# Kernel optimization log

Measured on AMD Instinct MI355X. Metric: run time of the kernel, lower is better.

## Reference

```python
import jax, jax.numpy as jnp
import numpy as np

RFF_DIM = 256
ATTENTION_SCALE = 0.1
LAMBDA_REG = 0.01
SIGMA = 1.0


def setup_inputs() -> dict:
    key = jax.random.key(0)
    k1, k2, k3 = jax.random.split(key, 3)
    N, D_IN = 262144, 64
    Z = jax.random.normal(k1, (N, D_IN), dtype=jnp.float32)
    W_rff = jax.random.normal(k2, (D_IN, RFF_DIM), dtype=jnp.float32)
    A = jax.random.normal(k3, (2 * RFF_DIM, 3), dtype=jnp.float32) * 0.01
    return {"Z": Z, "W_rff": W_rff, "A": A}


def reference(Z, W_rff, A):
    # --- RFF transform: Q = sqrt(1/R) * [cos(Z W / sigma), sin(Z W / sigma)] ---
    proj = (Z @ W_rff) / SIGMA                       # [N, R]
    Q = jnp.sqrt(1.0 / RFF_DIM) * jnp.concatenate(
        [jnp.cos(proj), jnp.sin(proj)], axis=-1)      # [N, 2R]

    N, F = Q.shape
    chunk = max(F // RFF_DIM, 1)                      # = 2 here
    n_chunks = F // chunk                             # = RFF_DIM

    # --- convexified attention over feature chunks (vectorized) ---
    Qc = Q.reshape(N, n_chunks, chunk)                # [N, K, c]
    A_mean = jnp.mean(A, axis=-1)                     # [2R]
    # per-chunk trace score: mean over batch of <Q_i, A_mean[:c]>
    scores = jnp.mean(jnp.einsum('nkc,c->nk', Qc, A_mean[:chunk]), axis=0)  # [K]
    alpha = jax.nn.softmax(scores / (ATTENTION_SCALE * np.sqrt(RFF_DIM)))   # [K]
    # per-chunk reweighting (dim-preserving recombination)
    Q_tilde = (alpha[None, :, None] * Qc).reshape(N, F)                      # [N, 2R]

    # --- small GEMM head + nuclear-norm regularizer ---
    predictions = Q_tilde @ A                          # [N, out]
    AW = jax.nn.softmax(predictions / np.sqrt(RFF_DIM), axis=-1)
    nuclear_norm = jnp.sum(jnp.linalg.svd(A, compute_uv=False))
    reg_loss = LAMBDA_REG * nuclear_norm
    return predictions, AW, reg_loss, alpha
```

## Files before the change

kernel.cpp:

```cpp
#include <hip/hip_runtime.h>
#include <math.h>

#define N_ROWS 262144
#define D_IN 64
#define RFF 256
#define NTILES (N_ROWS / 16)
#define GRID_BIG 1024
#define TILES_PER_BLOCK (NTILES / GRID_BIG)
#define TILES_PER_WAVE (TILES_PER_BLOCK / 4)

#define OFF_PRED 0
#define OFF_AW (N_ROWS * 3)
#define OFF_REG (2 * N_ROWS * 3)
#define OFF_ALPHA (2 * N_ROWS * 3 + 1)

#define WS_B 512
#define WS_WF 1280

typedef _Float16 f16x8 __attribute__((ext_vector_type(8)));
typedef float f32x4 __attribute__((ext_vector_type(4)));

__device__ __forceinline__ f32x4 mfma16(f16x8 a, f16x8 b, f32x4 c) {
    return __builtin_amdgcn_mfma_f32_16x16x32_f16(a, b, c, 0, 0, 0);
}

__device__ __forceinline__ unsigned short f32_to_bf16_rne(float x) {
    unsigned int u = __float_as_uint(x);
    unsigned int r = u + 0x7fffu + ((u >> 16) & 1u);
    return (unsigned short)(r >> 16);
}

__device__ __forceinline__ void gload_lds16(const float* g, float* lds) {
    __builtin_amdgcn_global_load_lds(
        (const __attribute__((address_space(1))) unsigned int*)g,
        (__attribute__((address_space(3))) unsigned int*)(lds), 16, 0, 0);
}

#define WAITVM0() do { asm volatile("s_waitcnt vmcnt(0)" ::: "memory"); \
                       __builtin_amdgcn_sched_barrier(0); } while (0)
#define LGKM0()   do { asm volatile("s_waitcnt lgkmcnt(0)" ::: "memory"); \
                       __builtin_amdgcn_sched_barrier(0); } while (0)

__global__ __launch_bounds__(256) void k_prep(const float* __restrict__ W,
                                              float* __restrict__ ws) {
    const int e = blockIdx.x * 256 + threadIdx.x;
    const int lane = e & 63;
    const int slot = e >> 6;
    const int kh = slot & 1;
    const int ct = slot >> 1;
    const int k0 = kh * 32 + 8 * (lane >> 4);
    const int col = ct * 16 + (lane & 15);
    f16x8 v;
#pragma unroll
    for (int i = 0; i < 8; ++i) v[i] = (_Float16)W[(k0 + i) * RFF + col];
    *(f16x8*)(ws + WS_WF + e * 4) = v;
}

__device__ __forceinline__ void dma_Bf(const float* __restrict__ wsWf, float* Bff,
                                       int wv, int l) {
#pragma unroll
    for (int m = 0; m < 8; ++m) {
        const int off = wv * 2048 + m * 256;
        gload_lds16(wsWf + off + l * 4, Bff + off);
    }
}

__device__ __forceinline__ void stage_dma(const float* __restrict__ Z, int n0, int l,
                                          float* ldsbase) {
#pragma unroll
    for (int m = 0; m < 4; ++m) {
        const int row = m * 4 + (l >> 4);
        const int gc = (l & 15) ^ (row & 7);
        gload_lds16(Z + (size_t)(n0 + row) * D_IN + gc * 4, ldsbase + m * 256);
    }
}

__device__ __forceinline__ void frags_from_lds(const float* bb, int lr, int lh,
                                               f16x8& ah0, f16x8& ah1) {
    const int s4 = lr & 7;
    const float* rp = bb + lr * 64;
    float z[16];
    *(float4*)&z[0]  = *(const float4*)(rp + (((lh * 2 + 0) ^ s4) << 2));
    *(float4*)&z[4]  = *(const float4*)(rp + (((lh * 2 + 1) ^ s4) << 2));
    *(float4*)&z[8]  = *(const float4*)(rp + (((lh * 2 + 8) ^ s4) << 2));
    *(float4*)&z[12] = *(const float4*)(rp + (((lh * 2 + 9) ^ s4) << 2));
    LGKM0();
#pragma unroll
    for (int i = 0; i < 8; ++i) {
        ah0[i] = (_Float16)z[i];
        ah1[i] = (_Float16)z[8 + i];
    }
}

__global__ __launch_bounds__(256, 3) void k_pass1(const float* __restrict__ Z,
                                                  const float* __restrict__ ws_in,
                                                  float* __restrict__ U) {
    __shared__ float Bff[8192];
    __shared__ float Zs[4][1024];
    __shared__ float Ured[512];
    const int t = threadIdx.x;
    const int wv = t >> 6, l = t & 63, lr = l & 15, lh = l >> 4;

    dma_Bf(ws_in + WS_WF, Bff, wv, l);
    const int tile0 = blockIdx.x * TILES_PER_BLOCK + wv * TILES_PER_WAVE;
    stage_dma(Z, tile0 * 16, l, &Zs[wv][0]);
    Ured[t] = 0.f;
    Ured[t + 256] = 0.f;
    __syncthreads();

    const f16x8* Bf = (const f16x8*)Bff;
    float accC[16], accS[16];
#pragma unroll
    for (int c = 0; c < 16; ++c) { accC[c] = 0.f; accS[c] = 0.f; }

#pragma unroll
    for (int tt = 0; tt < TILES_PER_WAVE; ++tt) {
        if (tt) WAITVM0();
        f16x8 ah0, ah1;
        frags_from_lds(&Zs[wv][0], lr, lh, ah0, ah1);
        if (tt + 1 < TILES_PER_WAVE) {
            stage_dma(Z, (tile0 + tt + 1) * 16, l, &Zs[wv][0]);
            __builtin_amdgcn_sched_barrier(0);
        }
        f32x4 acc[16];
#pragma unroll
        for (int ct = 0; ct < 16; ++ct) acc[ct] = (f32x4){0.f, 0.f, 0.f, 0.f};
#pragma unroll
        for (int ct = 0; ct < 16; ++ct) {
            acc[ct] = mfma16(ah0, Bf[(ct * 2 + 0) * 64 + l], acc[ct]);
            acc[ct] = mfma16(ah1, Bf[(ct * 2 + 1) * 64 + l], acc[ct]);
        }
#pragma unroll
        for (int ct = 0; ct < 16; ++ct) {
#pragma unroll
            for (int r = 0; r < 4; ++r) {
                float sn, cs;
                __sincosf(acc[ct][r], &sn, &cs);
                accC[ct] += cs;
                accS[ct] += sn;
            }
        }
    }
#pragma unroll
    for (int ct = 0; ct < 16; ++ct) {
        accC[ct] += __shfl_xor(accC[ct], 16);
        accC[ct] += __shfl_xor(accC[ct], 32);
        accS[ct] += __shfl_xor(accS[ct], 16);
        accS[ct] += __shfl_xor(accS[ct], 32);
    }
    if (l < 16) {
#pragma unroll
        for (int ct = 0; ct < 16; ++ct) {
            atomicAdd(&Ured[ct * 16 + l], accC[ct] * 0.0625f);
            atomicAdd(&Ured[256 + ct * 16 + l], accS[ct] * 0.0625f);
        }
    }
    __syncthreads();
    atomicAdd(&U[t], Ured[t]);
    atomicAdd(&U[t + 256], Ured[t + 256]);
}

__global__ __launch_bounds__(256) void k_alpha(const float* __restrict__ U,
                                               const float* __restrict__ A,
                                               float* __restrict__ ws,
                                               float* __restrict__ out) {
    __shared__ float sm[256];
    __shared__ double gred[256];
    __shared__ double G6[6];
    const int k = threadIdx.x;

    const float am0 = (A[0] + A[1] + A[2]) * (1.0f / 3.0f);
    const float am1 = (A[3] + A[4] + A[5]) * (1.0f / 3.0f);
    float score = (am0 * U[2 * k] + am1 * U[2 * k + 1]) * (1.0f / (float)N_ROWS);
    float x = score * (1.0f / 1.6f);

    sm[k] = x;
    __syncthreads();
    for (int s = 128; s > 0; s >>= 1) {
        if (k < s) sm[k] = fmaxf(sm[k], sm[k + s]);
        __syncthreads();
    }
    float mx = sm[0];
    __syncthreads();
    float e = __expf(x - mx);
    sm[k] = e;
    __syncthreads();
    for (int s = 128; s > 0; s >>= 1) {
        if (k < s) sm[k] += sm[k + s];
        __syncthreads();
    }
    float al = e / sm[0];
    out[OFF_ALPHA + k] = al;
    sm[k] = al;
    __syncthreads();

    {
        const float ac = 0.0625f * sm[k >> 1];
        const float as = 0.0625f * sm[128 + (k >> 1)];
        unsigned int* BtP = (unsigned int*)(ws + WS_B);
#pragma unroll
        for (int j = 0; j < 3; ++j) {
            float bc = ac * A[k * 3 + j];
            float bs = as * A[(256 + k) * 3 + j];
            unsigned int ulo = f32_to_bf16_rne(bc);
            unsigned int uhi = f32_to_bf16_rne(bs);
            BtP[k * 3 + j] = ulo | (uhi << 16);
        }
    }

    double af[2][3];
#pragma unroll
    for (int t2 = 0; t2 < 2; ++t2)
#pragma unroll
        for (int j = 0; j < 3; ++j) af[t2][j] = (double)A[(k + t2 * 256) * 3 + j];
    const int ei[6] = {0, 0, 0, 1, 1, 2};
    const int ej[6] = {0, 1, 2, 1, 2, 2};
    for (int eidx = 0; eidx < 6; ++eidx) {
        double p = af[0][ei[eidx]] * af[0][ej[eidx]] + af[1][ei[eidx]] * af[1][ej[eidx]];
        gred[k] = p;
        __syncthreads();
        for (int s = 128; s > 0; s >>= 1) {
            if (k < s) gred[k] += gred[k + s];
            __syncthreads();
        }
        if (k == 0) G6[eidx] = gred[0];
        __syncthreads();
    }
    if (k == 0) {
        double g00 = G6[0], g01 = G6[1], g02 = G6[2], g11 = G6[3], g12 = G6[4], g22 = G6[5];
        double q = (g00 + g11 + g22) / 3.0;
        double p1 = g01 * g01 + g02 * g02 + g12 * g12;
        double p2 = (g00 - q) * (g00 - q) + (g11 - q) * (g11 - q) + (g22 - q) * (g22 - q) + 2.0 * p1;
        double nuc;
        if (p2 < 1e-300) {
            nuc = 3.0 * sqrt(fmax(q, 0.0));
        } else {
            double p = sqrt(p2 / 6.0);
            double b00 = (g00 - q) / p, b11 = (g11 - q) / p, b22 = (g22 - q) / p;
            double b01 = g01 / p, b02 = g02 / p, b12 = g12 / p;
            double detB = b00 * (b11 * b22 - b12 * b12) - b01 * (b01 * b22 - b12 * b02) +
                          b02 * (b01 * b12 - b11 * b02);
            double rr = detB / 2.0;
            rr = fmin(1.0, fmax(-1.0, rr));
            double phi = acos(rr) / 3.0;
            double e1 = q + 2.0 * p * cos(phi);
            double e3 = q + 2.0 * p * cos(phi + 2.0943951023931953);
            double e2 = 3.0 * q - e1 - e3;
            nuc = sqrt(fmax(e1, 0.0)) + sqrt(fmax(e2, 0.0)) + sqrt(fmax(e3, 0.0));
        }
        out[OFF_REG] = (float)(0.01 * nuc);
    }
}

__global__ __launch_bounds__(256, 3) void k_pass2(const float* __restrict__ Z,
                                                  const float* __restrict__ ws_in,
                                                  float* __restrict__ out) {
    __shared__ float Bff[8192];
    __shared__ float Zs[4][1024];
    __shared__ unsigned int BtP[768];
    const int t = threadIdx.x;
    const int wv = t >> 6, l = t & 63, lr = l & 15, lh = l >> 4;

    dma_Bf(ws_in + WS_WF, Bff, wv, l);
    const int tile0 = blockIdx.x * TILES_PER_BLOCK + wv * TILES_PER_WAVE;
    stage_dma(Z, tile0 * 16, l, &Zs[wv][0]);
    {
        const unsigned int* src = (const unsigned int*)(ws_in + WS_B);
        BtP[t] = src[t];
        BtP[t + 256] = src[t + 256];
        BtP[t + 512] = src[t + 512];
    }
    __syncthreads();

    const f16x8* Bf = (const f16x8*)Bff;

#pragma unroll
    for (int tt = 0; tt < TILES_PER_WAVE; ++tt) {
        const int n0 = (tile0 + tt) * 16;
        if (tt) WAITVM0();
        f16x8 ah0, ah1;
        frags_from_lds(&Zs[wv][0], lr, lh, ah0, ah1);
        if (tt + 1 < TILES_PER_WAVE) {
            stage_dma(Z, (tile0 + tt + 1) * 16, l, &Zs[wv][0]);
            __builtin_amdgcn_sched_barrier(0);
        }
        f32x4 acc[16];
#pragma unroll
        for (int ct = 0; ct < 16; ++ct) acc[ct] = (f32x4){0.f, 0.f, 0.f, 0.f};
#pragma unroll
        for (int ct = 0; ct < 16; ++ct) {
            acc[ct] = mfma16(ah0, Bf[(ct * 2 + 0) * 64 + l], acc[ct]);
            acc[ct] = mfma16(ah1, Bf[(ct * 2 + 1) * 64 + l], acc[ct]);
        }
        float pa[4][3];
#pragma unroll
        for (int r = 0; r < 4; ++r) { pa[r][0] = 0.f; pa[r][1] = 0.f; pa[r][2] = 0.f; }
#pragma unroll
        for (int ct = 0; ct < 16; ++ct) {
            const int f = ct * 16 + lr;
            unsigned int u0 = BtP[f * 3 + 0], u1 = BtP[f * 3 + 1], u2 = BtP[f * 3 + 2];
            float bc0 = __uint_as_float(u0 << 16), bs0 = __uint_as_float(u0 & 0xffff0000u);
            float bc1 = __uint_as_float(u1 << 16), bs1 = __uint_as_float(u1 & 0xffff0000u);
            float bc2 = __uint_as_float(u2 << 16), bs2 = __uint_as_float(u2 & 0xffff0000u);
#pragma unroll
            for (int r = 0; r < 4; ++r) {
                float sn, cs;
                __sincosf(acc[ct][r], &sn, &cs);
                pa[r][0] = __builtin_fmaf(cs, bc0, __builtin_fmaf(sn, bs0, pa[r][0]));
                pa[r][1] = __builtin_fmaf(cs, bc1, __builtin_fmaf(sn, bs1, pa[r][1]));
                pa[r][2] = __builtin_fmaf(cs, bc2, __builtin_fmaf(sn, bs2, pa[r][2]));
            }
        }
#pragma unroll
        for (int r = 0; r < 4; ++r)
#pragma unroll
            for (int j = 0; j < 3; ++j) {
                pa[r][j] += __shfl_xor(pa[r][j], 1);
                pa[r][j] += __shfl_xor(pa[r][j], 2);
                pa[r][j] += __shfl_xor(pa[r][j], 4);
                pa[r][j] += __shfl_xor(pa[r][j], 8);
            }
        float q0 = 0.f, q1 = 0.f, q2 = 0.f;
#pragma unroll
        for (int r = 0; r < 4; ++r)
            if (lr == r) { q0 = pa[r][0]; q1 = pa[r][1]; q2 = pa[r][2]; }
        if (lr < 4) {
            const size_t n = (size_t)n0 + 4 * lh + lr;
            out[OFF_PRED + n * 3 + 0] = q0;
            out[OFF_PRED + n * 3 + 1] = q1;
            out[OFF_PRED + n * 3 + 2] = q2;
            float x0 = q0 * 0.0625f, x1 = q1 * 0.0625f, x2 = q2 * 0.0625f;
            float m = fmaxf(x0, fmaxf(x1, x2));
            float e0 = __expf(x0 - m), e1 = __expf(x1 - m), e2 = __expf(x2 - m);
            float inv = 1.0f / (e0 + e1 + e2);
            out[OFF_AW + n * 3 + 0] = e0 * inv;
            out[OFF_AW + n * 3 + 1] = e1 * inv;
            out[OFF_AW + n * 3 + 2] = e2 * inv;
        }
    }
}

extern "C" void kernel_launch(void* const* d_in, const int* in_sizes, int n_in,
                              void* d_out, int out_size, void* d_ws, size_t ws_size,
                              hipStream_t stream) {
    const float* Z = (const float*)d_in[0];
    const float* W = (const float*)d_in[1];
    const float* A = (const float*)d_in[2];
    float* out = (float*)d_out;
    float* ws = (float*)d_ws;

    (void)hipMemsetAsync(ws, 0, 512 * sizeof(float), stream);
    hipLaunchKernelGGL(k_prep, dim3(8), dim3(256), 0, stream, W, ws);
    hipLaunchKernelGGL(k_pass1, dim3(GRID_BIG), dim3(256), 0, stream, Z, ws, ws);
    hipLaunchKernelGGL(k_alpha, dim3(1), dim3(256), 0, stream, ws, A, ws, out);
    hipLaunchKernelGGL(k_pass2, dim3(GRID_BIG), dim3(256), 0, stream, Z, ws, out);
}
```

Baseline: 99.50 us.

## Use hardware revolution-based sincos, packed FMAs, rebalanced grid, fold memset into prep

Pre-scales W by 1/(2π) so that the projection is in revolutions, then uses v_fract + v_sin/v_cos directly instead of __sincosf, which removes the range-reduction cost. Accumulations and the head FMAs move to packed float2 vector ops. The grid shrinks to 768 blocks (3 per CU at 256 CUs), with uneven 5 or 6 tiles per wave, and the tile loops are no longer unrolled. The workspace memset is folded into k_prep to save a launch. Risks include fp16 precision of the scaled W and the loss of full unrolling.

```diff
diff --git a/kernel.cpp b/kernel.cpp
--- a/kernel.cpp
+++ b/kernel.cpp
@@ -5,9 +5,8 @@
 #define D_IN 64
 #define RFF 256
 #define NTILES (N_ROWS / 16)
-#define GRID_BIG 1024
-#define TILES_PER_BLOCK (NTILES / GRID_BIG)
-#define TILES_PER_WAVE (TILES_PER_BLOCK / 4)
+#define GRID_BIG 768
+#define NWAVES (GRID_BIG * 4)
 
 #define OFF_PRED 0
 #define OFF_AW (N_ROWS * 3)
@@ -19,6 +18,7 @@
 
 typedef _Float16 f16x8 __attribute__((ext_vector_type(8)));
 typedef float f32x4 __attribute__((ext_vector_type(4)));
+typedef float f32x2 __attribute__((ext_vector_type(2)));
 
 __device__ __forceinline__ f32x4 mfma16(f16x8 a, f16x8 b, f32x4 c) {
     return __builtin_amdgcn_mfma_f32_16x16x32_f16(a, b, c, 0, 0, 0);
@@ -30,6 +30,13 @@
     return (unsigned short)(r >> 16);
 }
 
+__device__ __forceinline__ void sincos_rev(float pr, float& sn, float& cs) {
+    float f;
+    asm("v_fract_f32 %0, %1" : "=v"(f) : "v"(pr));
+    asm("v_sin_f32 %0, %1" : "=v"(sn) : "v"(f));
+    asm("v_cos_f32 %0, %1" : "=v"(cs) : "v"(f));
+}
+
 __device__ __forceinline__ void gload_lds16(const float* g, float* lds) {
     __builtin_amdgcn_global_load_lds(
         (const __attribute__((address_space(1))) unsigned int*)g,
@@ -44,6 +51,7 @@
 __global__ __launch_bounds__(256) void k_prep(const float* __restrict__ W,
                                               float* __restrict__ ws) {
     const int e = blockIdx.x * 256 + threadIdx.x;
+    if (e < 512) ws[e] = 0.f;
     const int lane = e & 63;
     const int slot = e >> 6;
     const int kh = slot & 1;
@@ -52,7 +60,8 @@
     const int col = ct * 16 + (lane & 15);
     f16x8 v;
 #pragma unroll
-    for (int i = 0; i < 8; ++i) v[i] = (_Float16)W[(k0 + i) * RFF + col];
+    for (int i = 0; i < 8; ++i)
+        v[i] = (_Float16)(W[(k0 + i) * RFF + col] * 0.15915494309189535f);
     *(f16x8*)(ws + WS_WF + e * 4) = v;
 }
 
@@ -102,24 +111,25 @@
     const int wv = t >> 6, l = t & 63, lr = l & 15, lh = l >> 4;
 
     dma_Bf(ws_in + WS_WF, Bff, wv, l);
-    const int tile0 = blockIdx.x * TILES_PER_BLOCK + wv * TILES_PER_WAVE;
-    stage_dma(Z, tile0 * 16, l, &Zs[wv][0]);
+    const int gwid = blockIdx.x * 4 + wv;
+    const int tstart = gwid * 5 + (gwid < 1024 ? gwid : 1024);
+    const int tcnt = 5 + (gwid < 1024 ? 1 : 0);
+    stage_dma(Z, tstart * 16, l, &Zs[wv][0]);
     Ured[t] = 0.f;
     Ured[t + 256] = 0.f;
     __syncthreads();
 
     const f16x8* Bf = (const f16x8*)Bff;
-    float accC[16], accS[16];
-#pragma unroll
-    for (int c = 0; c < 16; ++c) { accC[c] = 0.f; accS[c] = 0.f; }
-
-#pragma unroll
-    for (int tt = 0; tt < TILES_PER_WAVE; ++tt) {
+    f32x2 accC2[16], accS2[16];
+#pragma unroll
+    for (int c = 0; c < 16; ++c) { accC2[c] = (f32x2){0.f, 0.f}; accS2[c] = (f32x2){0.f, 0.f}; }
+
+    for (int tt = 0; tt < tcnt; ++tt) {
         if (tt) WAITVM0();
         f16x8 ah0, ah1;
         frags_from_lds(&Zs[wv][0], lr, lh, ah0, ah1);
-        if (tt + 1 < TILES_PER_WAVE) {
-            stage_dma(Z, (tile0 + tt + 1) * 16, l, &Zs[wv][0]);
+        if (tt + 1 < tcnt) {
+            stage_dma(Z, (tstart + tt + 1) * 16, l, &Zs[wv][0]);
             __builtin_amdgcn_sched_barrier(0);
         }
         f32x4 acc[16];
@@ -132,27 +142,28 @@
         }
 #pragma unroll
         for (int ct = 0; ct < 16; ++ct) {
-#pragma unroll
-            for (int r = 0; r < 4; ++r) {
-                float sn, cs;
-                __sincosf(acc[ct][r], &sn, &cs);
-                accC[ct] += cs;
-                accS[ct] += sn;
-            }
+            float sn0, cs0, sn1, cs1, sn2, cs2, sn3, cs3;
+            sincos_rev(acc[ct][0], sn0, cs0);
+            sincos_rev(acc[ct][1], sn1, cs1);
+            sincos_rev(acc[ct][2], sn2, cs2);
+            sincos_rev(acc[ct][3], sn3, cs3);
+            accC2[ct] += (f32x2){cs0, cs1};
+            accC2[ct] += (f32x2){cs2, cs3};
+            accS2[ct] += (f32x2){sn0, sn1};
+            accS2[ct] += (f32x2){sn2, sn3};
         }
     }
 #pragma unroll
     for (int ct = 0; ct < 16; ++ct) {
-        accC[ct] += __shfl_xor(accC[ct], 16);
-        accC[ct] += __shfl_xor(accC[ct], 32);
-        accS[ct] += __shfl_xor(accS[ct], 16);
-        accS[ct] += __shfl_xor(accS[ct], 32);
-    }
-    if (l < 16) {
-#pragma unroll
-        for (int ct = 0; ct < 16; ++ct) {
-            atomicAdd(&Ured[ct * 16 + l], accC[ct] * 0.0625f);
-            atomicAdd(&Ured[256 + ct * 16 + l], accS[ct] * 0.0625f);
+        float c = accC2[ct][0] + accC2[ct][1];
+        float s = accS2[ct][0] + accS2[ct][1];
+        c += __shfl_xor(c, 16);
+        c += __shfl_xor(c, 32);
+        s += __shfl_xor(s, 16);
+        s += __shfl_xor(s, 32);
+        if (l < 16) {
+            atomicAdd(&Ured[ct * 16 + l], c * 0.0625f);
+            atomicAdd(&Ured[256 + ct * 16 + l], s * 0.0625f);
         }
     }
     __syncthreads();
@@ -262,8 +273,10 @@
     const int wv = t >> 6, l = t & 63, lr = l & 15, lh = l >> 4;
 
     dma_Bf(ws_in + WS_WF, Bff, wv, l);
-    const int tile0 = blockIdx.x * TILES_PER_BLOCK + wv * TILES_PER_WAVE;
-    stage_dma(Z, tile0 * 16, l, &Zs[wv][0]);
+    const int gwid = blockIdx.x * 4 + wv;
+    const int tstart = gwid * 5 + (gwid < 1024 ? gwid : 1024);
+    const int tcnt = 5 + (gwid < 1024 ? 1 : 0);
+    stage_dma(Z, tstart * 16, l, &Zs[wv][0]);
     {
         const unsigned int* src = (const unsigned int*)(ws_in + WS_B);
         BtP[t] = src[t];
@@ -274,14 +287,13 @@
 
     const f16x8* Bf = (const f16x8*)Bff;
 
-#pragma unroll
-    for (int tt = 0; tt < TILES_PER_WAVE; ++tt) {
-        const int n0 = (tile0 + tt) * 16;
+    for (int tt = 0; tt < tcnt; ++tt) {
+        const int n0 = (tstart + tt) * 16;
         if (tt) WAITVM0();
         f16x8 ah0, ah1;
         frags_from_lds(&Zs[wv][0], lr, lh, ah0, ah1);
-        if (tt + 1 < TILES_PER_WAVE) {
-            stage_dma(Z, (tile0 + tt + 1) * 16, l, &Zs[wv][0]);
+        if (tt + 1 < tcnt) {
+            stage_dma(Z, (tstart + tt + 1) * 16, l, &Zs[wv][0]);
             __builtin_amdgcn_sched_barrier(0);
         }
         f32x4 acc[16];
@@ -292,24 +304,42 @@
             acc[ct] = mfma16(ah0, Bf[(ct * 2 + 0) * 64 + l], acc[ct]);
             acc[ct] = mfma16(ah1, Bf[(ct * 2 + 1) * 64 + l], acc[ct]);
         }
-        float pa[4][3];
-#pragma unroll
-        for (int r = 0; r < 4; ++r) { pa[r][0] = 0.f; pa[r][1] = 0.f; pa[r][2] = 0.f; }
+        f32x2 pa01[3], pa23[3];
+#pragma unroll
+        for (int j = 0; j < 3; ++j) { pa01[j] = (f32x2){0.f, 0.f}; pa23[j] = (f32x2){0.f, 0.f}; }
 #pragma unroll
         for (int ct = 0; ct < 16; ++ct) {
             const int f = ct * 16 + lr;
             unsigned int u0 = BtP[f * 3 + 0], u1 = BtP[f * 3 + 1], u2 = BtP[f * 3 + 2];
-            float bc0 = __uint_as_float(u0 << 16), bs0 = __uint_as_float(u0 & 0xffff0000u);
-            float bc1 = __uint_as_float(u1 << 16), bs1 = __uint_as_float(u1 & 0xffff0000u);
-            float bc2 = __uint_as_float(u2 << 16), bs2 = __uint_as_float(u2 & 0xffff0000u);
-#pragma unroll
-            for (int r = 0; r < 4; ++r) {
-                float sn, cs;
-                __sincosf(acc[ct][r], &sn, &cs);
-                pa[r][0] = __builtin_fmaf(cs, bc0, __builtin_fmaf(sn, bs0, pa[r][0]));
-                pa[r][1] = __builtin_fmaf(cs, bc1, __builtin_fmaf(sn, bs1, pa[r][1]));
-                pa[r][2] = __builtin_fmaf(cs, bc2, __builtin_fmaf(sn, bs2, pa[r][2]));
+            float sn0, cs0, sn1, cs1, sn2, cs2, sn3, cs3;
+            sincos_rev(acc[ct][0], sn0, cs0);
+            sincos_rev(acc[ct][1], sn1, cs1);
+            sincos_rev(acc[ct][2], sn2, cs2);
+            sincos_rev(acc[ct][3], sn3, cs3);
+            const f32x2 cs01 = {cs0, cs1}, cs23 = {cs2, cs3};
+            const f32x2 sn01 = {sn0, sn1}, sn23 = {sn2, sn3};
+            const float bcf[3] = {__uint_as_float(u0 << 16), __uint_as_float(u1 << 16),
+                                  __uint_as_float(u2 << 16)};
+            const float bsf[3] = {__uint_as_float(u0 & 0xffff0000u),
+                                  __uint_as_float(u1 & 0xffff0000u),
+                                  __uint_as_float(u2 & 0xffff0000u)};
+#pragma unroll
+            for (int j = 0; j < 3; ++j) {
+                const f32x2 bc2 = {bcf[j], bcf[j]};
+                const f32x2 bs2 = {bsf[j], bsf[j]};
+                pa01[j] = __builtin_elementwise_fma(
+                    cs01, bc2, __builtin_elementwise_fma(sn01, bs2, pa01[j]));
+                pa23[j] = __builtin_elementwise_fma(
+                    cs23, bc2, __builtin_elementwise_fma(sn23, bs2, pa23[j]));
             }
+        }
+        float pa[4][3];
+#pragma unroll
+        for (int j = 0; j < 3; ++j) {
+            pa[0][j] = pa01[j][0];
+            pa[1][j] = pa01[j][1];
+            pa[2][j] = pa23[j][0];
+            pa[3][j] = pa23[j][1];
         }
 #pragma unroll
         for (int r = 0; r < 4; ++r)
@@ -349,7 +379,6 @@
     float* out = (float*)d_out;
     float* ws = (float*)d_ws;
 
-    (void)hipMemsetAsync(ws, 0, 512 * sizeof(float), stream);
     hipLaunchKernelGGL(k_prep, dim3(8), dim3(256), 0, stream, W, ws);
     hipLaunchKernelGGL(k_pass1, dim3(GRID_BIG), dim3(256), 0, stream, Z, ws, ws);
     hipLaunchKernelGGL(k_alpha, dim3(1), dim3(256), 0, stream, ws, A, ws, out);
```

Measured after the change: 88.82 us. 1.12x faster.
